# Kernel optimization log

Measured on AMD Instinct MI355X. Metric: run time of the kernel, lower is better.

The kernel has to match this reference:

```python
import jax, jax.numpy as jnp
import numpy as np

MSG_DIM = 100
REG_WEIGHT = 1.0
N_NODES = 100000
N_EDGES = 1000000
D_FEAT = 6
HIDDEN = 300
OUT_DIM = 2


def setup_inputs() -> dict:
    key = jax.random.key(0)
    ks = jax.random.split(key, 10)
    def glorot(k, shape):
        fan_in = shape[0]
        return jax.random.normal(k, shape, dtype=jnp.float32) / jnp.sqrt(jnp.float32(fan_in))
    return {
        "x": jax.random.normal(ks[0], (N_NODES, D_FEAT), dtype=jnp.float32),
        "edge_index": jax.random.randint(ks[1], (2, N_EDGES), 0, N_NODES, dtype=jnp.int64)
            if jax.config.jax_enable_x64 else jax.random.randint(ks[1], (2, N_EDGES), 0, N_NODES, dtype=jnp.int32),
        "y": jax.random.normal(ks[2], (N_NODES, OUT_DIM), dtype=jnp.float32),
        "target": jax.random.normal(ks[3], (N_NODES, OUT_DIM), dtype=jnp.float32),
        "W1": glorot(ks[4], (2 * D_FEAT, HIDDEN)),
        "b1": jnp.zeros((HIDDEN,), dtype=jnp.float32),
        "W2": glorot(ks[5], (HIDDEN, HIDDEN)),
        "b2": jnp.zeros((HIDDEN,), dtype=jnp.float32),
        "W3": glorot(ks[6], (HIDDEN, 2 * MSG_DIM)),
        "b3": jnp.zeros((2 * MSG_DIM,), dtype=jnp.float32),
    }


def reference(x, edge_index, y, target, W1, b1, W2, b2, W3, b3):
    # MAE term: sum |y - target| / n_nodes
    base_loss = jnp.sum(jnp.abs(y - target)) / y.shape[0]
    # Gather sender/receiver node features per edge and concat -> [E, 2*d_feat]
    e = jnp.concatenate([x[edge_index[0]], x[edge_index[1]]], axis=1)
    # edge_model MLP: 2*d_feat -> 300 -> 300 -> 2*msg_dim
    h = jax.nn.relu(e @ W1 + b1)
    h = jax.nn.relu(h @ W2 + b2)
    messages = h @ W3 + b3  # [E, 2*msg_dim]
    mu = messages[:, :MSG_DIM]
    logvar = messages[:, MSG_DIM:]
    kl_reg = jnp.sum(0.5 * (mu * mu + jnp.exp(logvar) - logvar - 1.0)) / messages.shape[0]
    return base_loss + REG_WEIGHT * kl_reg
```

## Files before the change

### kernel.cpp

```cpp
#include <hip/hip_runtime.h>

#define N_NODES 100000
#define N_EDGES 1000000
#define D_FEAT  6
#define HIDDEN  300
#define HID_P   320
#define MSG     100
#define OUTC    200
#define OUTC_P  208
#define MT      64
#define NT_H    (HID_P/16)
#define NT_M    (OUTC_P/16)
#define KS_H    (HID_P/32)

typedef __bf16 bf16_t;
typedef __bf16 bf16x8 __attribute__((ext_vector_type(8)));
typedef __bf16 bf16x4 __attribute__((ext_vector_type(4)));
typedef __bf16 bf16x2 __attribute__((ext_vector_type(2)));
typedef float  floatx4 __attribute__((ext_vector_type(4)));

#define PREP_BLOCKS 700
#define LOSS_BLOCKS 200
__global__ void prep_kernel(const float* __restrict__ W1, const float* __restrict__ W2,
                            const float* __restrict__ W3, bf16_t* __restrict__ W1P,
                            bf16_t* __restrict__ W2P, bf16_t* __restrict__ W3P,
                            const float* __restrict__ y, const float* __restrict__ t,
                            float* __restrict__ out) {
    if (blockIdx.x >= PREP_BLOCKS) {
        float s = 0.f;
        for (int i = (blockIdx.x - PREP_BLOCKS) * blockDim.x + threadIdx.x;
             i < N_NODES * 2; i += LOSS_BLOCKS * blockDim.x)
            s += fabsf(y[i] - t[i]);
        #pragma unroll
        for (int off = 32; off; off >>= 1) s += __shfl_down(s, off);
        __shared__ float red[4];
        if ((threadIdx.x & 63) == 0) red[threadIdx.x >> 6] = s;
        __syncthreads();
        if (threadIdx.x == 0)
            atomicAdd(out, (red[0] + red[1] + red[2] + red[3]) * (1.0f / N_NODES));
        return;
    }
    const int n1 = NT_H * 512;
    const int n2 = NT_H * KS_H * 512;
    const int n3 = NT_M * KS_H * 512;
    const int total = n1 + n2 + n3;
    for (int id = blockIdx.x * blockDim.x + threadIdx.x; id < total;
         id += PREP_BLOCKS * blockDim.x) {
        if (id < n1) {
            int nt = id >> 9, rem = id & 511, lane = rem >> 3, j = rem & 7;
            int n = nt * 16 + (lane & 15), k = (lane >> 4) * 8 + j;
            float v = (n < HIDDEN && k < 2 * D_FEAT) ? W1[k * HIDDEN + n] : 0.f;
            W1P[id] = (bf16_t)v;
        } else if (id < n1 + n2) {
            int r = id - n1;
            int chunk = r >> 9, rem = r & 511, lane = rem >> 3, j = rem & 7;
            int ks = chunk % KS_H, nt = chunk / KS_H;
            int n = nt * 16 + (lane & 15), k = ks * 32 + (lane >> 4) * 8 + j;
            float v = (n < HIDDEN && k < HIDDEN) ? W2[k * HIDDEN + n] : 0.f;
            W2P[r] = (bf16_t)v;
        } else {
            int r = id - n1 - n2;
            int chunk = r >> 9, rem = r & 511, lane = rem >> 3, j = rem & 7;
            int ks = chunk % KS_H, nt = chunk / KS_H;
            int n = nt * 16 + (lane & 15), k = ks * 32 + (lane >> 4) * 8 + j;
            float v = (n < OUTC && k < HIDDEN) ? W3[k * OUTC + n] : 0.f;
            W3P[r] = (bf16_t)v;
        }
    }
}

static __device__ __forceinline__ floatx4 mfma16(bf16x8 a, bf16x8 b, floatx4 c) {
    return __builtin_amdgcn_mfma_f32_16x16x32_bf16(a, b, c, 0, 0, 0);
}

template<int PE0, int KSN, int SE>
__device__ __forceinline__ void gemm_phase(
    const bf16_t* __restrict__ Wp, const bf16_t* __restrict__ Hsrc, int lane,
    int ntA, int ntB, int ntP,
    floatx4 (&aA)[4], floatx4 (&aB)[4], floatx4 (&aP)[2]) {
    #pragma unroll
    for (int e = 0; e < 4; e++) {
        aA[e] = (floatx4){0.f, 0.f, 0.f, 0.f};
        aB[e] = (floatx4){0.f, 0.f, 0.f, 0.f};
    }
    aP[0] = (floatx4){0.f, 0.f, 0.f, 0.f};
    aP[1] = (floatx4){0.f, 0.f, 0.f, 0.f};
    #pragma unroll 2
    for (int ks = 0; ks < KSN; ks++) {
        const bf16_t* wb = Wp + ks * 512 + lane * 8;
        bf16x8 wfA = *(const bf16x8*)(wb + ntA * (KSN * 512));
        bf16x8 wfB = *(const bf16x8*)(wb + ntB * (KSN * 512));
        bf16x8 wfP = *(const bf16x8*)(wb + ntP * (KSN * 512));
        const bf16_t* hb = Hsrc + ks * 512 + lane * 8;
        bf16x8 h0 = *(const bf16x8*)(hb + 0 * SE);
        aA[0] = mfma16(wfA, h0, aA[0]);
        aB[0] = mfma16(wfB, h0, aB[0]);
        if (PE0 == 0) aP[0] = mfma16(wfP, h0, aP[0]);
        bf16x8 h1 = *(const bf16x8*)(hb + 1 * SE);
        aA[1] = mfma16(wfA, h1, aA[1]);
        aB[1] = mfma16(wfB, h1, aB[1]);
        if (PE0 == 0) aP[1] = mfma16(wfP, h1, aP[1]);
        bf16x8 h2 = *(const bf16x8*)(hb + 2 * SE);
        aA[2] = mfma16(wfA, h2, aA[2]);
        aB[2] = mfma16(wfB, h2, aB[2]);
        if (PE0 == 2) aP[0] = mfma16(wfP, h2, aP[0]);
        bf16x8 h3 = *(const bf16x8*)(hb + 3 * SE);
        aA[3] = mfma16(wfA, h3, aA[3]);
        aB[3] = mfma16(wfB, h3, aB[3]);
        if (PE0 == 2) aP[1] = mfma16(wfP, h3, aP[1]);
    }
}

template<int NE>
__device__ __forceinline__ void epi_job(
    bf16_t* __restrict__ Hf, const float* __restrict__ bias,
    int nt, int q, int l16, int e0, const floatx4 (&acc)[NE]) {
    int n0 = nt * 16 + 4 * q;
    floatx4 bv = (n0 < HIDDEN) ? *(const floatx4*)&bias[n0]
                               : (floatx4){0.f, 0.f, 0.f, 0.f};
    int ks = n0 >> 5, lp = l16 + 16 * ((n0 >> 3) & 3), j0 = n0 & 7;
    #pragma unroll
    for (int p = 0; p < NE; p++) {
        bf16x4 pk;
        #pragma unroll
        for (int r = 0; r < 4; r++)
            pk[r] = (bf16_t)fmaxf(acc[p][r] + bv[r], 0.f);
        *(bf16x4*)&Hf[(((e0 + p) * KS_H + ks) * 64 + lp) * 8 + j0] = pk;
    }
}

template<int PE0>
__device__ __forceinline__ void epi_h(
    bf16_t* __restrict__ Hf, const float* __restrict__ bias, int q, int l16,
    int ntA, int ntB, int ntP,
    const floatx4 (&aA)[4], const floatx4 (&aB)[4], const floatx4 (&aP)[2]) {
    epi_job<4>(Hf, bias, ntA, q, l16, 0, aA);
    epi_job<4>(Hf, bias, ntB, q, l16, 0, aB);
    epi_job<2>(Hf, bias, ntP, q, l16, PE0, aP);
}

__global__ __launch_bounds__(512, 6) void mlp_kernel(
    const float* __restrict__ x, const int* __restrict__ ei,
    const bf16_t* __restrict__ W1P, const bf16_t* __restrict__ W2P,
    const bf16_t* __restrict__ W3P,
    const float* __restrict__ b1, const float* __restrict__ b2,
    const float* __restrict__ b3, float* __restrict__ out) {
    __shared__ __align__(16) bf16_t A1f[4 * 64 * 8];
    __shared__ __align__(16) bf16_t Hf[4 * KS_H * 64 * 8];
    __shared__ float red[8];

    const int tid  = threadIdx.x;
    const int w    = tid >> 6, lane = tid & 63;
    const int q    = lane >> 4, l16 = lane & 15;
    const long e0 = (long)blockIdx.x * MT;

    const int base = (10 * w) >> 2;
    const int ntA = (w & 1) ? base + 1 : base;
    const int ntB = (w & 1) ? base + 2 : base + 1;
    const int ntP = (w & 1) ? base     : base + 2;

    *(ulong*)&A1f[tid * 4] = 0ul;
    __syncthreads();
    if (tid < 2 * MT) {
        int m = tid >> 1, side = tid & 1;
        int node = ei[(long)side * N_EDGES + e0 + m];
        const float2* xr = (const float2*)(x + (long)node * D_FEAT);
        float2 v0 = xr[0], v1 = xr[1], v2 = xr[2];
        int et = m >> 4, ml = m & 15;
        bf16_t* Ab = &A1f[(et * 64 + ml) * 8];
        if (side == 0) {
            bf16x4 lo = {(bf16_t)v0.x, (bf16_t)v0.y, (bf16_t)v1.x, (bf16_t)v1.y};
            *(bf16x4*)&Ab[0] = lo;
            bf16x2 mid = {(bf16_t)v2.x, (bf16_t)v2.y};
            *(bf16x2*)&Ab[4] = mid;
        } else {
            bf16x2 hi2 = {(bf16_t)v0.x, (bf16_t)v0.y};
            *(bf16x2*)&Ab[6] = hi2;
            bf16x4 top = {(bf16_t)v1.x, (bf16_t)v1.y, (bf16_t)v2.x, (bf16_t)v2.y};
            *(bf16x4*)&A1f[(et * 64 + ml + 16) * 8] = top;
        }
    }
    __syncthreads();

    floatx4 aA[4], aB[4], aP[2];

    if (w & 1) {
        gemm_phase<2, 1, 512>(W1P, A1f, lane, ntA, ntB, ntP, aA, aB, aP);
        epi_h<2>(Hf, b1, q, l16, ntA, ntB, ntP, aA, aB, aP);
    } else {
        gemm_phase<0, 1, 512>(W1P, A1f, lane, ntA, ntB, ntP, aA, aB, aP);
        epi_h<0>(Hf, b1, q, l16, ntA, ntB, ntP, aA, aB, aP);
    }
    __syncthreads();

    if (w & 1)
        gemm_phase<2, KS_H, KS_H * 512>(W2P, Hf, lane, ntA, ntB, ntP, aA, aB, aP);
    else
        gemm_phase<0, KS_H, KS_H * 512>(W2P, Hf, lane, ntA, ntB, ntP, aA, aB, aP);
    __syncthreads();
    if (w & 1)
        epi_h<2>(Hf, b2, q, l16, ntA, ntB, ntP, aA, aB, aP);
    else
        epi_h<0>(Hf, b2, q, l16, ntA, ntB, ntP, aA, aB, aP);
    __syncthreads();

    const int cnt_m = (w >= 3) ? 2 : 1;
    floatx4 acc3[2][4];
    #pragma unroll
    for (int t = 0; t < 2; t++)
        #pragma unroll
        for (int e = 0; e < 4; e++) acc3[t][e] = (floatx4){0.f, 0.f, 0.f, 0.f};
    #pragma unroll 2
    for (int ks = 0; ks < KS_H; ks++) {
        bf16x8 hb[4];
        #pragma unroll
        for (int e = 0; e < 4; e++)
            hb[e] = *(const bf16x8*)&Hf[((e * KS_H + ks) * 64 + lane) * 8];
        #pragma unroll
        for (int t = 0; t < 2; t++) {
            if (t < cnt_m) {
                bf16x8 wf = *(const bf16x8*)&W3P[(((w + 5 * t) * KS_H + ks) * 64 + lane) * 8];
                #pragma unroll
                for (int e = 0; e < 4; e++)
                    acc3[t][e] = mfma16(wf, hb[e], acc3[t][e]);
            }
        }
    }
    float s = 0.f;
    #pragma unroll
    for (int t = 0; t < 2; t++) {
        if (t < cnt_m) {
            int n0 = (w + 5 * t) * 16 + 4 * q;
            if (n0 < OUTC) {
                floatx4 bv = *(const floatx4*)&b3[n0];
                bool is_mu = (n0 < MSG);
                #pragma unroll
                for (int e = 0; e < 4; e++)
                    #pragma unroll
                    for (int r = 0; r < 4; r++) {
                        float v = acc3[t][e][r] + bv[r];
                        if (is_mu) s += 0.5f * v * v;
                        else       s += 0.5f * (__expf(v) - v - 1.f);
                    }
            }
        }
    }
    #pragma unroll
    for (int off = 32; off; off >>= 1) s += __shfl_down(s, off);
    if (lane == 0) red[w] = s;
    __syncthreads();
    if (tid == 0) {
        float t2 = 0.f;
        #pragma unroll
        for (int i = 0; i < 8; i++) t2 += red[i];
        atomicAdd(out, t2 * (1.0f / N_EDGES));
    }
}

extern "C" void kernel_launch(void* const* d_in, const int* in_sizes, int n_in,
                              void* d_out, int out_size, void* d_ws, size_t ws_size,
                              hipStream_t stream) {
    const float* x      = (const float*)d_in[0];
    const int*   ei     = (const int*)d_in[1];
    const float* y      = (const float*)d_in[2];
    const float* target = (const float*)d_in[3];
    const float* W1     = (const float*)d_in[4];
    const float* b1     = (const float*)d_in[5];
    const float* W2     = (const float*)d_in[6];
    const float* b2     = (const float*)d_in[7];
    const float* W3     = (const float*)d_in[8];
    const float* b3     = (const float*)d_in[9];
    float* out = (float*)d_out;

    bf16_t* W1P = (bf16_t*)d_ws;
    bf16_t* W2P = W1P + NT_H * 512;
    bf16_t* W3P = W2P + NT_H * KS_H * 512;

    hipMemsetAsync(d_out, 0, sizeof(float), stream);
    prep_kernel<<<PREP_BLOCKS + LOSS_BLOCKS, 256, 0, stream>>>(
        W1, W2, W3, W1P, W2P, W3P, y, target, out);
    mlp_kernel<<<N_EDGES / MT, 512, 0, stream>>>(x, ei, W1P, W2P, W3P, b1, b2, b3, out);
}
```

Baseline: 443.2 us.

## Use 4 waves per block with 5x4 MFMA tiles per wave

Drops the block from 8 waves to 4. In the hidden layers each wave now computes 5 output column tiles across all 4 edge tiles, which gives more weight-fragment reuse per LDS H load and removes the uneven ntA/ntB/ntP split. The output layer gives each wave 3 full tiles plus one tile of the 13th column-tile across edge tiles. A1 zeroing is merged into the gather step, which removes one barrier. The trade-offs are fewer waves to hide latency and higher register pressure from 20 accumulators, with launch bounds changed to (256,3).

Measured after the change: 411.0 us. -7.3%, faster.

```diff
diff --git a/kernel.cpp b/kernel.cpp
--- a/kernel.cpp
+++ b/kernel.cpp
@@ -10,7 +10,7 @@
 #define OUTC_P  208
 #define MT      64
 #define NT_H    (HID_P/16)
-#define NT_M    (OUTC_P/16)
+#define NT_M    13
 #define KS_H    (HID_P/32)
 
 typedef __bf16 bf16_t;
@@ -73,73 +73,54 @@
     return __builtin_amdgcn_mfma_f32_16x16x32_bf16(a, b, c, 0, 0, 0);
 }
 
-template<int PE0, int KSN, int SE>
-__device__ __forceinline__ void gemm_phase(
-    const bf16_t* __restrict__ Wp, const bf16_t* __restrict__ Hsrc, int lane,
-    int ntA, int ntB, int ntP,
-    floatx4 (&aA)[4], floatx4 (&aB)[4], floatx4 (&aP)[2]) {
-    #pragma unroll
-    for (int e = 0; e < 4; e++) {
-        aA[e] = (floatx4){0.f, 0.f, 0.f, 0.f};
-        aB[e] = (floatx4){0.f, 0.f, 0.f, 0.f};
-    }
-    aP[0] = (floatx4){0.f, 0.f, 0.f, 0.f};
-    aP[1] = (floatx4){0.f, 0.f, 0.f, 0.f};
+template<int KSN, int SE>
+__device__ __forceinline__ void gemm5x4(
+    const bf16_t* __restrict__ Wbase0,
+    const bf16_t* __restrict__ Hsrc, int lane, floatx4 (&acc)[5][4]) {
+    #pragma unroll
+    for (int i = 0; i < 5; i++)
+        #pragma unroll
+        for (int e = 0; e < 4; e++) acc[i][e] = (floatx4){0.f, 0.f, 0.f, 0.f};
+    const bf16_t* Wb = Wbase0 + lane * 8;
+    const bf16_t* Hb = Hsrc + lane * 8;
     #pragma unroll 2
     for (int ks = 0; ks < KSN; ks++) {
-        const bf16_t* wb = Wp + ks * 512 + lane * 8;
-        bf16x8 wfA = *(const bf16x8*)(wb + ntA * (KSN * 512));
-        bf16x8 wfB = *(const bf16x8*)(wb + ntB * (KSN * 512));
-        bf16x8 wfP = *(const bf16x8*)(wb + ntP * (KSN * 512));
-        const bf16_t* hb = Hsrc + ks * 512 + lane * 8;
-        bf16x8 h0 = *(const bf16x8*)(hb + 0 * SE);
-        aA[0] = mfma16(wfA, h0, aA[0]);
-        aB[0] = mfma16(wfB, h0, aB[0]);
-        if (PE0 == 0) aP[0] = mfma16(wfP, h0, aP[0]);
-        bf16x8 h1 = *(const bf16x8*)(hb + 1 * SE);
-        aA[1] = mfma16(wfA, h1, aA[1]);
-        aB[1] = mfma16(wfB, h1, aB[1]);
-        if (PE0 == 0) aP[1] = mfma16(wfP, h1, aP[1]);
-        bf16x8 h2 = *(const bf16x8*)(hb + 2 * SE);
-        aA[2] = mfma16(wfA, h2, aA[2]);
-        aB[2] = mfma16(wfB, h2, aB[2]);
-        if (PE0 == 2) aP[0] = mfma16(wfP, h2, aP[0]);
-        bf16x8 h3 = *(const bf16x8*)(hb + 3 * SE);
-        aA[3] = mfma16(wfA, h3, aA[3]);
-        aB[3] = mfma16(wfB, h3, aB[3]);
-        if (PE0 == 2) aP[1] = mfma16(wfP, h3, aP[1]);
-    }
-}
-
-template<int NE>
-__device__ __forceinline__ void epi_job(
+        bf16x8 hb0 = *(const bf16x8*)(Hb + ks * 512);
+        bf16x8 hb1 = *(const bf16x8*)(Hb + ks * 512 + SE);
+        bf16x8 hb2 = *(const bf16x8*)(Hb + ks * 512 + 2 * SE);
+        bf16x8 hb3 = *(const bf16x8*)(Hb + ks * 512 + 3 * SE);
+        #pragma unroll
+        for (int i = 0; i < 5; i++) {
+            bf16x8 wf = *(const bf16x8*)(Wb + i * (KSN * 512) + ks * 512);
+            acc[i][0] = mfma16(wf, hb0, acc[i][0]);
+            acc[i][1] = mfma16(wf, hb1, acc[i][1]);
+            acc[i][2] = mfma16(wf, hb2, acc[i][2]);
+            acc[i][3] = mfma16(wf, hb3, acc[i][3]);
+        }
+    }
+}
+
+__device__ __forceinline__ void epi5(
     bf16_t* __restrict__ Hf, const float* __restrict__ bias,
-    int nt, int q, int l16, int e0, const floatx4 (&acc)[NE]) {
-    int n0 = nt * 16 + 4 * q;
-    floatx4 bv = (n0 < HIDDEN) ? *(const floatx4*)&bias[n0]
-                               : (floatx4){0.f, 0.f, 0.f, 0.f};
-    int ks = n0 >> 5, lp = l16 + 16 * ((n0 >> 3) & 3), j0 = n0 & 7;
-    #pragma unroll
-    for (int p = 0; p < NE; p++) {
-        bf16x4 pk;
-        #pragma unroll
-        for (int r = 0; r < 4; r++)
-            pk[r] = (bf16_t)fmaxf(acc[p][r] + bv[r], 0.f);
-        *(bf16x4*)&Hf[(((e0 + p) * KS_H + ks) * 64 + lp) * 8 + j0] = pk;
-    }
-}
-
-template<int PE0>
-__device__ __forceinline__ void epi_h(
-    bf16_t* __restrict__ Hf, const float* __restrict__ bias, int q, int l16,
-    int ntA, int ntB, int ntP,
-    const floatx4 (&aA)[4], const floatx4 (&aB)[4], const floatx4 (&aP)[2]) {
-    epi_job<4>(Hf, bias, ntA, q, l16, 0, aA);
-    epi_job<4>(Hf, bias, ntB, q, l16, 0, aB);
-    epi_job<2>(Hf, bias, ntP, q, l16, PE0, aP);
-}
-
-__global__ __launch_bounds__(512, 6) void mlp_kernel(
+    int w, int q, int l16, const floatx4 (&acc)[5][4]) {
+    #pragma unroll
+    for (int i = 0; i < 5; i++) {
+        int n0 = (5 * w + i) * 16 + 4 * q;
+        floatx4 bv = (n0 < HIDDEN) ? *(const floatx4*)&bias[n0]
+                                   : (floatx4){0.f, 0.f, 0.f, 0.f};
+        int ks = n0 >> 5, lp = l16 + 16 * ((n0 >> 3) & 3), j0 = n0 & 7;
+        #pragma unroll
+        for (int e = 0; e < 4; e++) {
+            bf16x4 pk;
+            #pragma unroll
+            for (int r = 0; r < 4; r++)
+                pk[r] = (bf16_t)fmaxf(acc[i][e][r] + bv[r], 0.f);
+            *(bf16x4*)&Hf[((e * KS_H + ks) * 64 + lp) * 8 + j0] = pk;
+        }
+    }
+}
+
+__global__ __launch_bounds__(256, 3) void mlp_kernel(
     const float* __restrict__ x, const int* __restrict__ ei,
     const bf16_t* __restrict__ W1P, const bf16_t* __restrict__ W2P,
     const bf16_t* __restrict__ W3P,
@@ -147,20 +128,13 @@
     const float* __restrict__ b3, float* __restrict__ out) {
     __shared__ __align__(16) bf16_t A1f[4 * 64 * 8];
     __shared__ __align__(16) bf16_t Hf[4 * KS_H * 64 * 8];
-    __shared__ float red[8];
+    __shared__ float red[4];
 
     const int tid  = threadIdx.x;
     const int w    = tid >> 6, lane = tid & 63;
     const int q    = lane >> 4, l16 = lane & 15;
     const long e0 = (long)blockIdx.x * MT;
 
-    const int base = (10 * w) >> 2;
-    const int ntA = (w & 1) ? base + 1 : base;
-    const int ntB = (w & 1) ? base + 2 : base + 1;
-    const int ntP = (w & 1) ? base     : base + 2;
-
-    *(ulong*)&A1f[tid * 4] = 0ul;
-    __syncthreads();
     if (tid < 2 * MT) {
         int m = tid >> 1, side = tid & 1;
         int node = ei[(long)side * N_EDGES + e0 + m];
@@ -176,72 +150,82 @@
         } else {
             bf16x2 hi2 = {(bf16_t)v0.x, (bf16_t)v0.y};
             *(bf16x2*)&Ab[6] = hi2;
-            bf16x4 top = {(bf16_t)v1.x, (bf16_t)v1.y, (bf16_t)v2.x, (bf16_t)v2.y};
-            *(bf16x4*)&A1f[(et * 64 + ml + 16) * 8] = top;
-        }
-    }
-    __syncthreads();
-
-    floatx4 aA[4], aB[4], aP[2];
-
-    if (w & 1) {
-        gemm_phase<2, 1, 512>(W1P, A1f, lane, ntA, ntB, ntP, aA, aB, aP);
-        epi_h<2>(Hf, b1, q, l16, ntA, ntB, ntP, aA, aB, aP);
+            bf16x8 top = {(bf16_t)v1.x, (bf16_t)v1.y, (bf16_t)v2.x, (bf16_t)v2.y,
+                          (bf16_t)0.f, (bf16_t)0.f, (bf16_t)0.f, (bf16_t)0.f};
+            *(bf16x8*)&A1f[(et * 64 + ml + 16) * 8] = top;
+        }
     } else {
-        gemm_phase<0, 1, 512>(W1P, A1f, lane, ntA, ntB, ntP, aA, aB, aP);
-        epi_h<0>(Hf, b1, q, l16, ntA, ntB, ntP, aA, aB, aP);
-    }
-    __syncthreads();
-
-    if (w & 1)
-        gemm_phase<2, KS_H, KS_H * 512>(W2P, Hf, lane, ntA, ntB, ntP, aA, aB, aP);
-    else
-        gemm_phase<0, KS_H, KS_H * 512>(W2P, Hf, lane, ntA, ntB, ntP, aA, aB, aP);
-    __syncthreads();
-    if (w & 1)
-        epi_h<2>(Hf, b2, q, l16, ntA, ntB, ntP, aA, aB, aP);
-    else
-        epi_h<0>(Hf, b2, q, l16, ntA, ntB, ntP, aA, aB, aP);
-    __syncthreads();
-
-    const int cnt_m = (w >= 3) ? 2 : 1;
-    floatx4 acc3[2][4];
-    #pragma unroll
-    for (int t = 0; t < 2; t++)
-        #pragma unroll
-        for (int e = 0; e < 4; e++) acc3[t][e] = (floatx4){0.f, 0.f, 0.f, 0.f};
-    #pragma unroll 2
-    for (int ks = 0; ks < KS_H; ks++) {
-        bf16x8 hb[4];
+        int idx = tid - 128;
+        int et = idx >> 5, lr = 32 + (idx & 31);
+        bf16x8 z = {};
+        *(bf16x8*)&A1f[(et * 64 + lr) * 8] = z;
+    }
+    __syncthreads();
+
+    floatx4 acc[5][4];
+
+    gemm5x4<1, 512>(W1P + (5 * w) * 512, A1f, lane, acc);
+    epi5(Hf, b1, w, q, l16, acc);
+    __syncthreads();
+
+    gemm5x4<KS_H, KS_H * 512>(W2P + (5 * w) * (KS_H * 512), Hf, lane, acc);
+    __syncthreads();
+    epi5(Hf, b2, w, q, l16, acc);
+    __syncthreads();
+
+    floatx4 a3[3][4], aq;
+    #pragma unroll
+    for (int t = 0; t < 3; t++)
+        #pragma unroll
+        for (int e = 0; e < 4; e++) a3[t][e] = (floatx4){0.f, 0.f, 0.f, 0.f};
+    aq = (floatx4){0.f, 0.f, 0.f, 0.f};
+    {
+        const bf16_t* W3b = W3P + (3 * w) * (KS_H * 512) + lane * 8;
+        const bf16_t* Wqb = W3P + 12 * (KS_H * 512) + lane * 8;
+        const bf16_t* Hb  = Hf + lane * 8;
+        const bf16_t* Hq  = Hf + w * (KS_H * 512) + lane * 8;
+        #pragma unroll 2
+        for (int ks = 0; ks < KS_H; ks++) {
+            bf16x8 hb0 = *(const bf16x8*)(Hb + ks * 512);
+            bf16x8 hb1 = *(const bf16x8*)(Hb + ks * 512 + KS_H * 512);
+            bf16x8 hb2 = *(const bf16x8*)(Hb + ks * 512 + 2 * KS_H * 512);
+            bf16x8 hb3 = *(const bf16x8*)(Hb + ks * 512 + 3 * KS_H * 512);
+            #pragma unroll
+            for (int t = 0; t < 3; t++) {
+                bf16x8 wf = *(const bf16x8*)(W3b + t * (KS_H * 512) + ks * 512);
+                a3[t][0] = mfma16(wf, hb0, a3[t][0]);
+                a3[t][1] = mfma16(wf, hb1, a3[t][1]);
+                a3[t][2] = mfma16(wf, hb2, a3[t][2]);
+                a3[t][3] = mfma16(wf, hb3, a3[t][3]);
+            }
+            bf16x8 wq = *(const bf16x8*)(Wqb + ks * 512);
+            bf16x8 hq = *(const bf16x8*)(Hq + ks * 512);
+            aq = mfma16(wq, hq, aq);
+        }
+    }
+    float s = 0.f;
+    #pragma unroll
+    for (int t = 0; t < 3; t++) {
+        int n0 = (3 * w + t) * 16 + 4 * q;
+        floatx4 bv = *(const floatx4*)&b3[n0];
+        bool is_mu = (n0 < MSG);
         #pragma unroll
         for (int e = 0; e < 4; e++)
-            hb[e] = *(const bf16x8*)&Hf[((e * KS_H + ks) * 64 + lane) * 8];
-        #pragma unroll
-        for (int t = 0; t < 2; t++) {
-            if (t < cnt_m) {
-                bf16x8 wf = *(const bf16x8*)&W3P[(((w + 5 * t) * KS_H + ks) * 64 + lane) * 8];
-                #pragma unroll
-                for (int e = 0; e < 4; e++)
-                    acc3[t][e] = mfma16(wf, hb[e], acc3[t][e]);
+            #pragma unroll
+            for (int r = 0; r < 4; r++) {
+                float v = a3[t][e][r] + bv[r];
+                if (is_mu) s += 0.5f * v * v;
+                else       s += 0.5f * (__expf(v) - v - 1.f);
             }
-        }
-    }
-    float s = 0.f;
-    #pragma unroll
-    for (int t = 0; t < 2; t++) {
-        if (t < cnt_m) {
-            int n0 = (w + 5 * t) * 16 + 4 * q;
-            if (n0 < OUTC) {
-                floatx4 bv = *(const floatx4*)&b3[n0];
-                bool is_mu = (n0 < MSG);
-                #pragma unroll
-                for (int e = 0; e < 4; e++)
-                    #pragma unroll
-                    for (int r = 0; r < 4; r++) {
-                        float v = acc3[t][e][r] + bv[r];
-                        if (is_mu) s += 0.5f * v * v;
-                        else       s += 0.5f * (__expf(v) - v - 1.f);
-                    }
+    }
+    {
+        int n0q = 192 + 4 * q;
+        if (n0q < OUTC) {
+            floatx4 bq = *(const floatx4*)&b3[n0q];
+            #pragma unroll
+            for (int r = 0; r < 4; r++) {
+                float v = aq[r] + bq[r];
+                s += 0.5f * (__expf(v) - v - 1.f);
             }
         }
     }
@@ -249,12 +233,8 @@
     for (int off = 32; off; off >>= 1) s += __shfl_down(s, off);
     if (lane == 0) red[w] = s;
     __syncthreads();
-    if (tid == 0) {
-        float t2 = 0.f;
-        #pragma unroll
-        for (int i = 0; i < 8; i++) t2 += red[i];
-        atomicAdd(out, t2 * (1.0f / N_EDGES));
-    }
+    if (tid == 0)
+        atomicAdd(out, (red[0] + red[1] + red[2] + red[3]) * (1.0f / N_EDGES));
 }
 
 extern "C" void kernel_launch(void* const* d_in, const int* in_sizes, int n_in,
@@ -279,5 +259,5 @@
     hipMemsetAsync(d_out, 0, sizeof(float), stream);
     prep_kernel<<<PREP_BLOCKS + LOSS_BLOCKS, 256, 0, stream>>>(
         W1, W2, W3, W1P, W2P, W3P, y, target, out);
-    mlp_kernel<<<N_EDGES / MT, 512, 0, stream>>>(x, ei, W1P, W2P, W3P, b1, b2, b3, out);
-}
+    mlp_kernel<<<N_EDGES / MT, 256, 0, stream>>>(x, ei, W1P, W2P, W3P, b1, b2, b3, out);
+}
```
